# Kernel tuning notes

Hardware: AMD Instinct MI355X
Metric: run time of the kernel (lower is better)

The kernel has to match this reference:

```python
import jax, jax.numpy as jnp
import numpy as np

B, P_LEN, Q_LEN, HID = 8, 2048, 1024, 1024


def setup_inputs() -> dict:
    key = jax.random.key(0)
    k1, k2, k3, k4 = jax.random.split(key, 4)
    k = jax.random.normal(k1, (B, P_LEN, HID), dtype=jnp.float32)
    q = jax.random.normal(k2, (B, Q_LEN, HID), dtype=jnp.float32)
    # q_mask: True = pad token. All-valid mask (no pads) to avoid NaN rows.
    q_mask = jnp.zeros((B, Q_LEN), dtype=bool)
    # Xavier-normal-initialized Linear weights, shape [out, in] as in torch.
    std = float(np.sqrt(2.0 / (HID + HID)))
    Wk = jax.random.normal(k3, (HID, HID), dtype=jnp.float32) * std
    Wq = jax.random.normal(k4, (HID, HID), dtype=jnp.float32) * std
    return {"k": k, "q": q, "q_mask": q_mask, "Wk": Wk, "Wq": Wq}


def reference(k, q, q_mask, Wk, Wq):
    # relu-projected keys/queries (Linear has no bias)
    p_key = jax.nn.relu(jnp.einsum('bpd,hd->bph', k, Wk))   # [B, p_len, hid]
    q_key = jax.nn.relu(jnp.einsum('bqd,hd->bqh', q, Wq))   # [B, q_len, hid]
    scores = jnp.einsum('bph,bqh->bpq', p_key, q_key)        # [B, p_len, q_len]
    scores = jnp.where(q_mask[:, None, :], -jnp.inf, scores)
    alphas = jax.nn.softmax(scores, axis=-1)                 # [B, p_len, q_len]
    ctx = jnp.einsum('bpq,bqd->bpd', alphas, q)              # [B, p_len, q_dim]
    return ctx, alphas
```

## Files before the change

kernel.cpp:

```cpp
#include <hip/hip_runtime.h>
#include <hip/hip_bf16.h>
#include <math.h>


typedef _Float16 v8h __attribute__((ext_vector_type(8)));
typedef _Float16 v4h __attribute__((ext_vector_type(4)));
typedef float v4f __attribute__((ext_vector_type(4)));

#define AS1C(p) ((const __attribute__((address_space(1))) void*)(p))
#define AS3(p)  ((__attribute__((address_space(3))) void*)(p))

__global__ __launch_bounds__(512) void gemm_nt_f16_256(
    const _Float16* __restrict__ A, const _Float16* __restrict__ B,
    float* __restrict__ Cf, _Float16* __restrict__ Ch,
    int N, int K, int Mtiles, int Ntiles,
    long long sA, long long sB, long long sC, int relu)
{
  extern __shared__ _Float16 lds[];

  const int nwg = gridDim.x;
  const int cpx = nwg >> 3;
  const int bid = (blockIdx.x & 7) * cpx + (blockIdx.x >> 3);
  const int mt  = bid % Mtiles;
  const int nt  = (bid / Mtiles) % Ntiles;
  const int bz  = bid / (Mtiles * Ntiles);

  A += (long long)bz * sA;
  B += (long long)bz * sB;

  const int m0 = mt * 256;
  const int n0 = nt * 256;
  const int t  = threadIdx.x;
  const int l  = t & 63;
  const int w  = t >> 6;
  const int wm = (w >> 2) * 128;
  const int wn = (w & 3) * 64;
  const int fr = l & 15;
  const int fq = l >> 4;

  const int tr = t >> 2;
  const int tc = (t & 3) * 8;

  const _Float16* A0 = A + (long long)(m0 + tr) * K + tc;
  const _Float16* A1 = A + (long long)(m0 + 128 + tr) * K + tc;
  const _Float16* B0 = B + (long long)(n0 + tr) * K + tc;
  const _Float16* B1 = B + (long long)(n0 + 128 + tr) * K + tc;

  v4f acc[8][4];
#pragma unroll
  for (int i = 0; i < 8; ++i)
#pragma unroll
    for (int j = 0; j < 4; ++j)
      acc[i][j] = (v4f){0.f, 0.f, 0.f, 0.f};

  const int NT = K >> 5;

#define STAGE(kt) do {                                                              \
    _Float16* s_ = lds + (((kt) & 3) << 14);                                        \
    const int ko_ = (kt) << 5;                                                      \
    __builtin_amdgcn_global_load_lds(AS1C(A0 + ko_), AS3(s_ +         t * 8), 16, 0, 0); \
    __builtin_amdgcn_global_load_lds(AS1C(A1 + ko_), AS3(s_ +  4096 + t * 8), 16, 0, 0); \
    __builtin_amdgcn_global_load_lds(AS1C(B0 + ko_), AS3(s_ +  8192 + t * 8), 16, 0, 0); \
    __builtin_amdgcn_global_load_lds(AS1C(B1 + ko_), AS3(s_ + 12288 + t * 8), 16, 0, 0); \
  } while (0)

  STAGE(0);
  STAGE(1);
  STAGE(2);

  for (int kt = 0; kt < NT; ++kt) {
    if (kt < NT - 2)       asm volatile("s_waitcnt vmcnt(8)" ::: "memory");
    else if (kt == NT - 2) asm volatile("s_waitcnt vmcnt(4)" ::: "memory");
    else                   asm volatile("s_waitcnt vmcnt(0)" ::: "memory");
    __builtin_amdgcn_sched_barrier(0);
    __builtin_amdgcn_s_barrier();
    asm volatile("" ::: "memory");

    if (kt + 3 < NT) STAGE(kt + 3);

    const _Float16* As_ = lds + ((kt & 3) << 14);
    const _Float16* Bs_ = As_ + 8192;

    v8h a[8], b[4];
#pragma unroll
    for (int i = 0; i < 8; ++i)
      a[i] = *(const v8h*)&As_[(wm + i * 16 + fr) * 32 + fq * 8];
#pragma unroll
    for (int j = 0; j < 4; ++j)
      b[j] = *(const v8h*)&Bs_[(wn + j * 16 + fr) * 32 + fq * 8];

    __builtin_amdgcn_s_setprio(1);
#pragma unroll
    for (int i = 0; i < 8; ++i)
#pragma unroll
      for (int j = 0; j < 4; ++j)
        acc[i][j] = __builtin_amdgcn_mfma_f32_16x16x32_f16(a[i], b[j], acc[i][j], 0, 0, 0);
    __builtin_amdgcn_s_setprio(0);
    asm volatile("s_waitcnt lgkmcnt(0)" ::: "memory");
    __builtin_amdgcn_sched_barrier(0);
  }
#undef STAGE

  float* Cfb = Cf ? Cf + (long long)bz * sC : nullptr;
  _Float16* Chb = Ch ? Ch + (long long)bz * sC : nullptr;
#pragma unroll
  for (int i = 0; i < 8; ++i) {
#pragma unroll
    for (int j = 0; j < 4; ++j) {
#pragma unroll
      for (int r = 0; r < 4; ++r) {
        const int row = m0 + wm + i * 16 + fq * 4 + r;
        const int col = n0 + wn + j * 16 + fr;
        float v = acc[i][j][r];
        if (relu) v = fmaxf(v, 0.f);
        if (Cfb) Cfb[(long long)row * N + col] = v;
        if (Chb) Chb[(long long)row * N + col] = (_Float16)v;
      }
    }
  }
}

__global__ __launch_bounds__(256) void convert_all_kernel(
    const float* __restrict__ s0, _Float16* __restrict__ d0, int b0,
    const float* __restrict__ s1, _Float16* __restrict__ d1, int b1,
    const float* __restrict__ s2, _Float16* __restrict__ d2, int b2,
    const float* __restrict__ s3, _Float16* __restrict__ d3)
{
  int blk = blockIdx.x;
  const float* src;
  _Float16* dst;
  if (blk < b0)           { src = s0; dst = d0; }
  else if (blk < b0 + b1) { src = s1; dst = d1; blk -= b0; }
  else if (blk < b0 + b1 + b2) { src = s2; dst = d2; blk -= b0 + b1; }
  else                    { src = s3; dst = d3; blk -= b0 + b1 + b2; }
  const long long i = ((long long)blk * 256 + threadIdx.x) * 4;
  const float4 v = *(const float4*)(src + i);
  v4h o = {(_Float16)v.x, (_Float16)v.y, (_Float16)v.z, (_Float16)v.w};
  *(v4h*)(dst + i) = o;
}

__global__ __launch_bounds__(256) void transpose_f16_kernel(
    const float* __restrict__ q, _Float16* __restrict__ qT, int Q, int H)
{
  __shared__ float tile[64][65];
  const float* qb = q + (long long)blockIdx.z * Q * H;
  _Float16* qTb = qT + (long long)blockIdx.z * H * Q;
  const int q0 = blockIdx.x * 64, h0 = blockIdx.y * 64;
  const int t = threadIdx.x;
  const int tr = t >> 4, tc = (t & 15) << 2;
#pragma unroll
  for (int i = 0; i < 4; ++i) {
    const float4 v = *(const float4*)(qb + (long long)(q0 + tr + i * 16) * H + h0 + tc);
    tile[tr + i * 16][tc + 0] = v.x;
    tile[tr + i * 16][tc + 1] = v.y;
    tile[tr + i * 16][tc + 2] = v.z;
    tile[tr + i * 16][tc + 3] = v.w;
  }
  __syncthreads();
#pragma unroll
  for (int i = 0; i < 4; ++i) {
    const int hl = tr + i * 16;
    const int ql = tc;
    v4h o = {(_Float16)tile[ql + 0][hl], (_Float16)tile[ql + 1][hl],
             (_Float16)tile[ql + 2][hl], (_Float16)tile[ql + 3][hl]};
    *(v4h*)(qTb + (long long)(h0 + hl) * Q + q0 + ql) = o;
  }
}

__global__ __launch_bounds__(256) void softmax_rows_kernel(
    float* __restrict__ S, _Float16* __restrict__ S16,
    const unsigned char* __restrict__ qmask, int Q, int P)
{
  const long long row = blockIdx.x;
  const int b = (int)(row / P);
  float* s = S + row * (long long)Q;
  const unsigned char* msk = qmask + (long long)b * Q;
  const int t = threadIdx.x;
  float4 v = *(const float4*)(s + (t << 2));
  float vals[4] = {v.x, v.y, v.z, v.w};
#pragma unroll
  for (int j = 0; j < 4; ++j)
    if (msk[(t << 2) + j]) vals[j] = -INFINITY;

  __shared__ float red[8];
  const int wid = t >> 6, lid = t & 63;

  float mx = fmaxf(fmaxf(vals[0], vals[1]), fmaxf(vals[2], vals[3]));
#pragma unroll
  for (int o = 32; o > 0; o >>= 1) mx = fmaxf(mx, __shfl_xor(mx, o, 64));
  if (lid == 0) red[wid] = mx;
  __syncthreads();
  mx = fmaxf(fmaxf(red[0], red[1]), fmaxf(red[2], red[3]));

  float e[4];
  float sum = 0.f;
#pragma unroll
  for (int j = 0; j < 4; ++j) { e[j] = __expf(vals[j] - mx); sum += e[j]; }
#pragma unroll
  for (int o = 32; o > 0; o >>= 1) sum += __shfl_xor(sum, o, 64);
  __syncthreads();
  if (lid == 0) red[4 + wid] = sum;
  __syncthreads();
  sum = red[4] + red[5] + red[6] + red[7];
  const float inv = 1.f / sum;

  float4 o;
  o.x = e[0] * inv; o.y = e[1] * inv; o.z = e[2] * inv; o.w = e[3] * inv;
  *(float4*)(s + (t << 2)) = o;
  v4h oh = {(_Float16)o.x, (_Float16)o.y, (_Float16)o.z, (_Float16)o.w};
  *(v4h*)(S16 + row * (long long)Q + (t << 2)) = oh;
}

extern "C" void kernel_launch(void* const* d_in, const int* in_sizes, int n_in,
                              void* d_out, int out_size, void* d_ws, size_t ws_size,
                              hipStream_t stream)
{
  const int B = 8, P = 2048, Q = 1024, H = 1024;
  const float* k  = (const float*)d_in[0];
  const float* q  = (const float*)d_in[1];
  const unsigned char* qmask = (const unsigned char*)d_in[2];
  const float* Wk = (const float*)d_in[3];
  const float* Wq = (const float*)d_in[4];

  float* ctx    = (float*)d_out;
  float* alphas = ctx + (size_t)B * P * H;

  _Float16* pkey16 = (_Float16*)d_out;

  char* wsb = (char*)d_ws;
  _Float16* qkey16   = (_Float16*)(wsb);
  _Float16* k16      = (_Float16*)(wsb + 16777216);
  _Float16* alphas16 = k16;
  _Float16* q16      = (_Float16*)(wsb + 16777216 + 33554432);
  _Float16* qT16     = q16;
  _Float16* Wk16     = (_Float16*)(wsb + 67108864);
  _Float16* Wq16     = (_Float16*)(wsb + 69206016);

  const long long nK = (long long)B * P * H;
  const long long nQ = (long long)B * Q * H;
  const long long nW = (long long)H * H;

  const int bK = (int)(nK / 1024), bQ = (int)(nQ / 1024), bW = (int)(nW / 1024);
  convert_all_kernel<<<bK + bQ + 2 * bW, 256, 0, stream>>>(
      k, k16, bK, q, q16, bQ, Wk, Wk16, bW, Wq, Wq16);

  const size_t LDSB = 131072;
  gemm_nt_f16_256<<<64 * 4, 512, LDSB, stream>>>(
      k16, Wk16, nullptr, pkey16, H, H, 64, 4, 0LL, 0LL, 0LL, 1);
  gemm_nt_f16_256<<<32 * 4, 512, LDSB, stream>>>(
      q16, Wq16, nullptr, qkey16, H, H, 32, 4, 0LL, 0LL, 0LL, 1);
  gemm_nt_f16_256<<<8 * 4 * B, 512, LDSB, stream>>>(
      pkey16, qkey16, alphas, nullptr, Q, H, 8, 4,
      (long long)P * H, (long long)Q * H, (long long)P * Q, 0);
  transpose_f16_kernel<<<dim3(Q / 64, H / 64, B), 256, 0, stream>>>(q, qT16, Q, H);
  softmax_rows_kernel<<<B * P, 256, 0, stream>>>(alphas, alphas16, qmask, Q, P);
  gemm_nt_f16_256<<<8 * 4 * B, 512, LDSB, stream>>>(
      alphas16, qT16, ctx, nullptr, H, Q, 8, 4,
      (long long)P * Q, (long long)H * Q, (long long)P * H, 0);
}
```

Baseline: 394.9 us.

## Switch GEMM to BK=64 double-buffered XOR-swizzled LDS with split fragment loads

The GEMM k-loop changes from a 4-stage BK=32 pipeline to a 2-stage BK=64 double buffer in the same LDS footprint. Rows are stored with an XOR swizzle on 16-byte chunks to avoid LDS bank conflicts. The MFMA work is split into four quadrants with interleaved fragment reloads to cut register pressure. This trades pipeline depth and adds a second barrier per iteration in exchange for fewer iterations and conflict-free LDS reads.

```diff
diff --git a/kernel.cpp b/kernel.cpp
--- a/kernel.cpp
+++ b/kernel.cpp
@@ -37,14 +37,15 @@
   const int wn = (w & 3) * 64;
   const int fr = l & 15;
   const int fq = l >> 4;
-
-  const int tr = t >> 2;
-  const int tc = (t & 3) * 8;
-
-  const _Float16* A0 = A + (long long)(m0 + tr) * K + tc;
-  const _Float16* A1 = A + (long long)(m0 + 128 + tr) * K + tc;
-  const _Float16* B0 = B + (long long)(n0 + tr) * K + tc;
-  const _Float16* B1 = B + (long long)(n0 + 128 + tr) * K + tc;
+  const int r3 = fr & 7;
+  const int sa0 = (fq ^ r3) * 8;
+  const int sa1 = ((4 + fq) ^ r3) * 8;
+
+  const int trow = t >> 3;
+  const int tswz = ((t & 7) ^ (trow & 7)) * 8;
+
+  const _Float16* Ast = A + (long long)(m0 + trow) * K + tswz;
+  const _Float16* Bst = B + (long long)(n0 + trow) * K + tswz;
 
   v4f acc[8][4];
 #pragma unroll
@@ -53,68 +54,122 @@
     for (int j = 0; j < 4; ++j)
       acc[i][j] = (v4f){0.f, 0.f, 0.f, 0.f};
 
-  const int NT = K >> 5;
-
-#define STAGE(kt) do {                                                              \
-    _Float16* s_ = lds + (((kt) & 3) << 14);                                        \
-    const int ko_ = (kt) << 5;                                                      \
-    __builtin_amdgcn_global_load_lds(AS1C(A0 + ko_), AS3(s_ +         t * 8), 16, 0, 0); \
-    __builtin_amdgcn_global_load_lds(AS1C(A1 + ko_), AS3(s_ +  4096 + t * 8), 16, 0, 0); \
-    __builtin_amdgcn_global_load_lds(AS1C(B0 + ko_), AS3(s_ +  8192 + t * 8), 16, 0, 0); \
-    __builtin_amdgcn_global_load_lds(AS1C(B1 + ko_), AS3(s_ + 12288 + t * 8), 16, 0, 0); \
+  const int NT = K >> 6;
+
+#define STAGE(kt) do {                                                                   \
+    _Float16* s_ = lds + (((kt) & 1) << 15);                                             \
+    const long long ko_ = (long long)((kt) << 6);                                        \
+    __builtin_amdgcn_global_load_lds(AS1C(Ast + ko_),                AS3(s_ +         t * 8), 16, 0, 0); \
+    __builtin_amdgcn_global_load_lds(AS1C(Ast +  64LL * K + ko_),    AS3(s_ +  4096 + t * 8), 16, 0, 0); \
+    __builtin_amdgcn_global_load_lds(AS1C(Ast + 128LL * K + ko_),    AS3(s_ +  8192 + t * 8), 16, 0, 0); \
+    __builtin_amdgcn_global_load_lds(AS1C(Ast + 192LL * K + ko_),    AS3(s_ + 12288 + t * 8), 16, 0, 0); \
+    __builtin_amdgcn_global_load_lds(AS1C(Bst + ko_),                AS3(s_ + 16384 + t * 8), 16, 0, 0); \
+    __builtin_amdgcn_global_load_lds(AS1C(Bst +  64LL * K + ko_),    AS3(s_ + 20480 + t * 8), 16, 0, 0); \
+    __builtin_amdgcn_global_load_lds(AS1C(Bst + 128LL * K + ko_),    AS3(s_ + 24576 + t * 8), 16, 0, 0); \
+    __builtin_amdgcn_global_load_lds(AS1C(Bst + 192LL * K + ko_),    AS3(s_ + 28672 + t * 8), 16, 0, 0); \
   } while (0)
 
   STAGE(0);
-  STAGE(1);
-  STAGE(2);
 
   for (int kt = 0; kt < NT; ++kt) {
-    if (kt < NT - 2)       asm volatile("s_waitcnt vmcnt(8)" ::: "memory");
-    else if (kt == NT - 2) asm volatile("s_waitcnt vmcnt(4)" ::: "memory");
-    else                   asm volatile("s_waitcnt vmcnt(0)" ::: "memory");
+    if (kt + 1 < NT) {
+      STAGE(kt + 1);
+      asm volatile("s_waitcnt vmcnt(8)" ::: "memory");
+    } else {
+      asm volatile("s_waitcnt vmcnt(0)" ::: "memory");
+    }
     __builtin_amdgcn_sched_barrier(0);
     __builtin_amdgcn_s_barrier();
     asm volatile("" ::: "memory");
 
-    if (kt + 3 < NT) STAGE(kt + 3);
-
-    const _Float16* As_ = lds + ((kt & 3) << 14);
-    const _Float16* Bs_ = As_ + 8192;
-
-    v8h a[8], b[4];
-#pragma unroll
-    for (int i = 0; i < 8; ++i)
-      a[i] = *(const v8h*)&As_[(wm + i * 16 + fr) * 32 + fq * 8];
-#pragma unroll
-    for (int j = 0; j < 4; ++j)
-      b[j] = *(const v8h*)&Bs_[(wn + j * 16 + fr) * 32 + fq * 8];
-
+    const _Float16* Ab = lds + ((kt & 1) << 15);
+    const _Float16* Bb = Ab + 16384;
+
+    v8h a0[4], a1[4], b0[4], b1[4];
+
+#pragma unroll
+    for (int i = 0; i < 4; ++i) {
+      a0[i] = *(const v8h*)&Ab[(wm + i * 16 + fr) * 64 + sa0];
+      a1[i] = *(const v8h*)&Ab[(wm + i * 16 + fr) * 64 + sa1];
+    }
+#pragma unroll
+    for (int j = 0; j < 2; ++j) {
+      b0[j] = *(const v8h*)&Bb[(wn + j * 16 + fr) * 64 + sa0];
+      b1[j] = *(const v8h*)&Bb[(wn + j * 16 + fr) * 64 + sa1];
+    }
     __builtin_amdgcn_s_setprio(1);
 #pragma unroll
-    for (int i = 0; i < 8; ++i)
-#pragma unroll
-      for (int j = 0; j < 4; ++j)
-        acc[i][j] = __builtin_amdgcn_mfma_f32_16x16x32_f16(a[i], b[j], acc[i][j], 0, 0, 0);
+    for (int i = 0; i < 4; ++i)
+#pragma unroll
+      for (int j = 0; j < 2; ++j) {
+        acc[i][j] = __builtin_amdgcn_mfma_f32_16x16x32_f16(a0[i], b0[j], acc[i][j], 0, 0, 0);
+        acc[i][j] = __builtin_amdgcn_mfma_f32_16x16x32_f16(a1[i], b1[j], acc[i][j], 0, 0, 0);
+      }
     __builtin_amdgcn_s_setprio(0);
+
+#pragma unroll
+    for (int j = 2; j < 4; ++j) {
+      b0[j] = *(const v8h*)&Bb[(wn + j * 16 + fr) * 64 + sa0];
+      b1[j] = *(const v8h*)&Bb[(wn + j * 16 + fr) * 64 + sa1];
+    }
+    __builtin_amdgcn_s_setprio(1);
+#pragma unroll
+    for (int i = 0; i < 4; ++i)
+#pragma unroll
+      for (int j = 2; j < 4; ++j) {
+        acc[i][j] = __builtin_amdgcn_mfma_f32_16x16x32_f16(a0[i], b0[j], acc[i][j], 0, 0, 0);
+        acc[i][j] = __builtin_amdgcn_mfma_f32_16x16x32_f16(a1[i], b1[j], acc[i][j], 0, 0, 0);
+      }
+    __builtin_amdgcn_s_setprio(0);
+
+#pragma unroll
+    for (int i = 0; i < 4; ++i) {
+      a0[i] = *(const v8h*)&Ab[(wm + 64 + i * 16 + fr) * 64 + sa0];
+      a1[i] = *(const v8h*)&Ab[(wm + 64 + i * 16 + fr) * 64 + sa1];
+    }
+    __builtin_amdgcn_s_setprio(1);
+#pragma unroll
+    for (int i = 0; i < 4; ++i)
+#pragma unroll
+      for (int j = 2; j < 4; ++j) {
+        acc[4 + i][j] = __builtin_amdgcn_mfma_f32_16x16x32_f16(a0[i], b0[j], acc[4 + i][j], 0, 0, 0);
+        acc[4 + i][j] = __builtin_amdgcn_mfma_f32_16x16x32_f16(a1[i], b1[j], acc[4 + i][j], 0, 0, 0);
+      }
+    __builtin_amdgcn_s_setprio(0);
+
+    __builtin_amdgcn_s_setprio(1);
+#pragma unroll
+    for (int i = 0; i < 4; ++i)
+#pragma unroll
+      for (int j = 0; j < 2; ++j) {
+        acc[4 + i][j] = __builtin_amdgcn_mfma_f32_16x16x32_f16(a0[i], b0[j], acc[4 + i][j], 0, 0, 0);
+        acc[4 + i][j] = __builtin_amdgcn_mfma_f32_16x16x32_f16(a1[i], b1[j], acc[4 + i][j], 0, 0, 0);
+      }
+    __builtin_amdgcn_s_setprio(0);
+
     asm volatile("s_waitcnt lgkmcnt(0)" ::: "memory");
     __builtin_amdgcn_sched_barrier(0);
+    __builtin_amdgcn_s_barrier();
   }
 #undef STAGE
 
   float* Cfb = Cf ? Cf + (long long)bz * sC : nullptr;
   _Float16* Chb = Ch ? Ch + (long long)bz * sC : nullptr;
 #pragma unroll
-  for (int i = 0; i < 8; ++i) {
-#pragma unroll
-    for (int j = 0; j < 4; ++j) {
-#pragma unroll
-      for (int r = 0; r < 4; ++r) {
-        const int row = m0 + wm + i * 16 + fq * 4 + r;
-        const int col = n0 + wn + j * 16 + fr;
-        float v = acc[i][j][r];
-        if (relu) v = fmaxf(v, 0.f);
-        if (Cfb) Cfb[(long long)row * N + col] = v;
-        if (Chb) Chb[(long long)row * N + col] = (_Float16)v;
+  for (int mh = 0; mh < 2; ++mh) {
+#pragma unroll
+    for (int i = 0; i < 4; ++i) {
+#pragma unroll
+      for (int j = 0; j < 4; ++j) {
+#pragma unroll
+        for (int r = 0; r < 4; ++r) {
+          const int row = m0 + wm + mh * 64 + i * 16 + fq * 4 + r;
+          const int col = n0 + wn + j * 16 + fr;
+          float v = acc[mh * 4 + i][j][r];
+          if (relu) v = fmaxf(v, 0.f);
+          if (Cfb) Cfb[(long long)row * N + col] = v;
+          if (Chb) Chb[(long long)row * N + col] = (_Float16)v;
+        }
       }
     }
   }
```

Result: no change. 387.4 us (-1.9%).
